# Optimization experiments

Hardware: AMD Instinct MI355X
Metric: run time of the kernel (lower is better)

Reference implementation:

```python
import jax, jax.numpy as jnp
import numpy as np

B, S, D, H = 4, 2048, 1024, 16
DK = D // H
THETA = 10000.0


def _rope(x, token_positions):
    # x: [b, h, s, d_k]; token_positions: [s] int
    half = x.shape[-1] // 2
    freqs = 1.0 / (THETA ** (2.0 * jnp.arange(half, dtype=jnp.float32) / x.shape[-1]))
    angles = token_positions.astype(jnp.float32)[:, None] * freqs[None, :]  # [s, half]
    cos, sin = jnp.cos(angles), jnp.sin(angles)
    x1 = x[..., 0::2]  # interleaved pairing: (d/2, 2)
    x2 = x[..., 1::2]
    r1 = x1 * cos - x2 * sin
    r2 = x2 * cos + x1 * sin
    return jnp.stack([r1, r2], axis=-1).reshape(x.shape)


def setup_inputs() -> dict:
    key = jax.random.key(0)
    ks = jax.random.split(key, 5)
    std_io = np.sqrt(2.0 / (D + D)).astype(np.float32)
    return {
        "x": jax.random.normal(ks[0], (B, S, D), dtype=jnp.float32),
        "token_positions": jnp.arange(S, dtype=jnp.int32),
        "Wq": jax.random.normal(ks[1], (D, D), dtype=jnp.float32) * std_io,
        "Wk": jax.random.normal(ks[2], (D, D), dtype=jnp.float32) * std_io,
        "Wv": jax.random.normal(ks[3], (D, D), dtype=jnp.float32) * std_io,
        "Wo": jax.random.normal(ks[4], (D, D), dtype=jnp.float32) * std_io,
    }


def reference(x, token_positions, Wq, Wk, Wv, Wo):
    b, s, d = x.shape
    # Linear uses W: [out, in] -> y = x @ W.T
    def proj(W):
        y = jnp.einsum('bsd,od->bso', x, W)
        return y.reshape(b, s, H, DK).transpose(0, 2, 1, 3)  # [b,h,s,dk]
    q, k, v = proj(Wq), proj(Wk), proj(Wv)
    q = _rope(q, token_positions)
    k = _rope(k, token_positions)
    scores = jnp.einsum('bhqd,bhkd->bhqk', q, k) / jnp.sqrt(jnp.float32(DK))
    causal = jnp.tril(jnp.ones((s, s), dtype=bool))
    scores = jnp.where(causal, scores, -jnp.inf)
    attn = jax.nn.softmax(scores, axis=-1)
    out = jnp.einsum('bhqk,bhkd->bhqd', attn, v)
    out = out.transpose(0, 2, 1, 3).reshape(b, s, d)
    return jnp.einsum('bsd,od->bso', out, Wo)
```

## Files before the change

### kernel.cpp

```cpp
#include <hip/hip_runtime.h>
#include <math.h>

#define B_ 4
#define S_ 2048
#define D_ 1024
#define H_ 16
#define DK_ 64
#define SCALE_ 0.125f
#define THETA_ 10000.0f
#define LOG2E_ 1.44269504f
#define THR_ 8.0f

typedef unsigned short ushort_t;
typedef __attribute__((ext_vector_type(8))) short bf16x8;
typedef __attribute__((ext_vector_type(4))) float f32x4;

__device__ __forceinline__ ushort_t f2bf(float f) {
    union { float f; unsigned u; } v; v.f = f;
    unsigned r = (v.u + 0x7FFFu + ((v.u >> 16) & 1u)) >> 16;
    return (ushort_t)r;
}

__device__ __forceinline__ unsigned permpk(float lo, float hi) {
    return __builtin_amdgcn_perm(__float_as_uint(hi), __float_as_uint(lo), 0x07060302u);
}

__device__ __forceinline__ int vswz(int row) { return (row & 7) ^ ((row >> 3) & 3); }

#define GLOAD_LDS16(gptr, lptr)                                                   \
    __builtin_amdgcn_global_load_lds(                                             \
        (const __attribute__((address_space(1))) unsigned int*)(gptr),            \
        (__attribute__((address_space(3))) unsigned int*)(lptr), 16, 0, 0)

__global__ __launch_bounds__(256) void cast_f32_bf16(const float* __restrict__ in,
                                                     ushort_t* __restrict__ out, int n) {
    int i = (blockIdx.x * 256 + threadIdx.x) * 4;
    if (i >= n) return;
    float4 v = *reinterpret_cast<const float4*>(in + i);
    unsigned lo = (unsigned)f2bf(v.x) | ((unsigned)f2bf(v.y) << 16);
    unsigned hi = (unsigned)f2bf(v.z) | ((unsigned)f2bf(v.w) << 16);
    uint2 u; u.x = lo; u.y = hi;
    *reinterpret_cast<uint2*>(out + i) = u;
}

__global__ __launch_bounds__(256) void build_rope(const int* __restrict__ pos,
                                                  float2* __restrict__ tab) {
    int i = blockIdx.x * 256 + threadIdx.x;
    int s = i >> 5, p = i & 31;
    float freq = powf(THETA_, -2.0f * (float)p / 64.0f);
    float a = (float)pos[s] * freq;
    tab[i] = make_float2(cosf(a), sinf(a));
}

template <int MODE>
__global__ __launch_bounds__(256) void gemm_bf16(const ushort_t* __restrict__ A,
                                                 const ushort_t* __restrict__ W,
                                                 const float2* __restrict__ tab,
                                                 float qscale,
                                                 float* __restrict__ outF,
                                                 ushort_t* __restrict__ outB) {
    __shared__ ushort_t Asl[128 * 32];
    __shared__ ushort_t Bsl[128 * 32];

    const int t = threadIdx.x;
    const int lane = t & 63;
    const int w = t >> 6;
    const int lr = lane & 15;
    const int lg = lane >> 4;

    const int bid = blockIdx.x;
    const int swz = (bid & 7) * 64 + (bid >> 3);
    const int m0 = (swz >> 3) * 128;
    const int n0 = (swz & 7) * 128;

    const int wr = w >> 1;
    const int wc = w & 1;

    f32x4 acc[4][4] = {};

    for (int k0 = 0; k0 < D_; k0 += 32) {
#pragma unroll
        for (int i = 0; i < 2; ++i) {
            const int off = w * 2048 + i * 1024 + lane * 16;
            const int row = off >> 6;
            const int col = (off & 63) >> 1;
            GLOAD_LDS16(A + (size_t)(m0 + row) * D_ + k0 + col, Asl + (w * 1024 + i * 512));
            GLOAD_LDS16(W + (size_t)(n0 + row) * D_ + k0 + col, Bsl + (w * 1024 + i * 512));
        }
        __syncthreads();

        bf16x8 af[4], bfr[4];
#pragma unroll
        for (int x = 0; x < 4; ++x) {
            af[x]  = *reinterpret_cast<const bf16x8*>(&Asl[(wr * 64 + x * 16 + lr) * 32 + lg * 8]);
            bfr[x] = *reinterpret_cast<const bf16x8*>(&Bsl[(wc * 64 + x * 16 + lr) * 32 + lg * 8]);
        }
#pragma unroll
        for (int mi = 0; mi < 4; ++mi)
#pragma unroll
            for (int ni = 0; ni < 4; ++ni)
                acc[mi][ni] = __builtin_amdgcn_mfma_f32_16x16x32_bf16(af[mi], bfr[ni], acc[mi][ni], 0, 0, 0);
        __syncthreads();
    }

#pragma unroll
    for (int mi = 0; mi < 4; ++mi) {
#pragma unroll
        for (int r = 0; r < 4; ++r) {
            const int m = m0 + wr * 64 + mi * 16 + lg * 4 + r;
            const int bb = m >> 11;
            const int s = m & (S_ - 1);
#pragma unroll
            for (int ni = 0; ni < 4; ++ni) {
                const int n = n0 + wc * 64 + ni * 16 + lr;
                float v = acc[mi][ni][r];
                if (MODE == 0) {
                    outF[(size_t)m * D_ + n] = v;
                } else {
                    const int h = n >> 6, dk = n & 63;
                    if (MODE == 2) {
                        v *= qscale;
                        const float2 cs = tab[s * 32 + (dk >> 1)];
                        const float part = __shfl_xor(v, 1, 64);
                        v = (dk & 1) ? fmaf(v, cs.x, part * cs.y)
                                     : fmaf(v, cs.x, -part * cs.y);
                    }
                    outB[(((size_t)bb * H_ + h) * S_ + s) * DK_ + dk] = f2bf(v);
                }
            }
        }
    }
}

__global__ __launch_bounds__(256) void attn_mfma(const ushort_t* __restrict__ Q,
                                                 const ushort_t* __restrict__ K,
                                                 const ushort_t* __restrict__ V,
                                                 ushort_t* __restrict__ O) {
    __shared__ ushort_t Ks[2][64 * 64];
    __shared__ ushort_t Vt[64 * 64];
    __shared__ ushort_t Pl[64 * 64];

    const int t = threadIdx.x;
    const int lane = t & 63;
    const int w = t >> 6;
    const int lr = lane & 15;
    const int lg = lane >> 4;

    const int bid = blockIdx.x;
    const int swz = (bid & 7) * 128 + (bid >> 3);
    const int bh = swz >> 4;
    const int p  = swz & 15;

    const ushort_t* Kbase = K + (size_t)bh * S_ * DK_;
    const ushort_t* Vbase = V + (size_t)bh * S_ * DK_;
    const int bb = bh >> 4, h = bh & 15;

    const int dk8 = (t & 7) * 8;
    const int kv2 = (t >> 3) * 2;

    bf16x8 ones;
#pragma unroll
    for (int j = 0; j < 8; ++j) ones[j] = (short)0x3F80;

    bf16x8 vpre0, vpre1;

    for (int ph = 0; ph < 2; ++ph) {
        const int qt = ph ? (31 - p) : p;
        const int q0 = qt * 64;
        const int nt = qt + 1;

        const ushort_t* Qbase = Q + ((size_t)bh * S_ + q0 + w * 16) * DK_;
        bf16x8 qf[2];
#pragma unroll
        for (int kf = 0; kf < 2; ++kf)
            qf[kf] = *reinterpret_cast<const bf16x8*>(
                Qbase + (size_t)lr * DK_ + kf * 32 + lg * 8);

        f32x4 acc[4] = {};
        f32x4 accl = {};
        float mrow = -INFINITY;

#pragma unroll
        for (int it = 0; it < 2; ++it) {
            const int slotbase = w * 64 + it * 256;
            const int slot = slotbase + lane;
            const int row = slot >> 3;
            const int c16 = (slot & 7) ^ (row & 7);
            GLOAD_LDS16(Kbase + (size_t)row * DK_ + c16 * 8, &Ks[0][slotbase * 8]);
        }
        {
            const ushort_t* Vsrc = Vbase + (size_t)kv2 * DK_ + dk8;
            vpre0 = *reinterpret_cast<const bf16x8*>(Vsrc);
            vpre1 = *reinterpret_cast<const bf16x8*>(Vsrc + DK_);
        }
        __syncthreads();

        int cur = 0;
        for (int kt = 0; kt < nt; ++kt) {
            {
                const unsigned* aw = reinterpret_cast<const unsigned*>(&vpre0);
                const unsigned* bw = reinterpret_cast<const unsigned*>(&vpre1);
#pragma unroll
                for (int j = 0; j < 8; ++j) {
                    const int row = dk8 + j;
                    const unsigned sel = (j & 1) ? 0x07060302u : 0x05040100u;
                    const unsigned pk = __builtin_amdgcn_perm(bw[j >> 1], aw[j >> 1], sel);
                    *reinterpret_cast<unsigned*>(
                        (char*)Vt + row * 128 + ((kv2 * 2) ^ (vswz(row) << 4))) = pk;
                }
            }
            __syncthreads();

            if (kt + 1 < nt) {
                const ushort_t* Ksrc = Kbase + (size_t)(kt + 1) * 64 * DK_;
#pragma unroll
                for (int it = 0; it < 2; ++it) {
                    const int slotbase = w * 64 + it * 256;
                    const int slot = slotbase + lane;
                    const int row = slot >> 3;
                    const int c16 = (slot & 7) ^ (row & 7);
                    GLOAD_LDS16(Ksrc + (size_t)row * DK_ + c16 * 8, &Ks[cur ^ 1][slotbase * 8]);
                }
                const ushort_t* Vsrc = Vbase + (size_t)((kt + 1) * 64 + kv2) * DK_ + dk8;
                vpre0 = *reinterpret_cast<const bf16x8*>(Vsrc);
                vpre1 = *reinterpret_cast<const bf16x8*>(Vsrc + DK_);
            }

            bf16x8 kb[4][2];
#pragma unroll
            for (int nf = 0; nf < 4; ++nf)
#pragma unroll
                for (int kf = 0; kf < 2; ++kf)
                    kb[nf][kf] = *reinterpret_cast<const bf16x8*>(
                        (char*)Ks[cur] + (nf * 16 + lr) * 128 + (((kf * 4 + lg) ^ (lr & 7)) << 4));

            f32x4 sT[4];
#pragma unroll
            for (int nf = 0; nf < 4; ++nf) {
                f32x4 z = {};
                z = __builtin_amdgcn_mfma_f32_16x16x32_bf16(kb[nf][0], qf[0], z, 0, 0, 0);
                z = __builtin_amdgcn_mfma_f32_16x16x32_bf16(kb[nf][1], qf[1], z, 0, 0, 0);
                sT[nf] = z;
            }

            if (kt == nt - 1) {
                const int q = q0 + w * 16 + lr;
#pragma unroll
                for (int nf = 0; nf < 4; ++nf)
#pragma unroll
                    for (int r = 0; r < 4; ++r) {
                        const int kv = kt * 64 + nf * 16 + lg * 4 + r;
                        if (kv > q) sT[nf][r] = -INFINITY;
                    }
            }

            {
                float m4 = -INFINITY;
#pragma unroll
                for (int nf = 0; nf < 4; ++nf)
#pragma unroll
                    for (int r = 0; r < 4; ++r) m4 = fmaxf(m4, sT[nf][r]);
                m4 = fmaxf(m4, __shfl_xor(m4, 16, 64));
                m4 = fmaxf(m4, __shfl_xor(m4, 32, 64));
                if (m4 > mrow + THR_) {
                    const float corr = __builtin_amdgcn_exp2f(mrow - m4);
                    mrow = m4;
#pragma unroll
                    for (int r = 0; r < 4; ++r) accl[r] *= corr;
#pragma unroll
                    for (int df = 0; df < 4; ++df)
#pragma unroll
                        for (int r = 0; r < 4; ++r) acc[df][r] *= corr;
                }
            }

            const int prow = w * 16 + lr;
            char* prowp = (char*)Pl + prow * 128;
#pragma unroll
            for (int nf = 0; nf < 4; ++nf) {
                const float p0 = __builtin_amdgcn_exp2f(sT[nf][0] - mrow);
                const float p1 = __builtin_amdgcn_exp2f(sT[nf][1] - mrow);
                const float p2 = __builtin_amdgcn_exp2f(sT[nf][2] - mrow);
                const float p3 = __builtin_amdgcn_exp2f(sT[nf][3] - mrow);
                uint2 pk;
                pk.x = permpk(p0, p1);
                pk.y = permpk(p2, p3);
                const int chunk = (nf * 2 + (lg >> 1)) ^ (lr & 7);
                *reinterpret_cast<uint2*>(prowp + (chunk << 4) + (lg & 1) * 8) = pk;
            }

            bf16x8 pfr[2];
#pragma unroll
            for (int kf = 0; kf < 2; ++kf)
                pfr[kf] = *reinterpret_cast<const bf16x8*>(
                    (char*)Pl + prow * 128 + (((kf * 4 + lg) ^ (lr & 7)) << 4));

            bf16x8 vtf[4][2];
#pragma unroll
            for (int df = 0; df < 4; ++df)
#pragma unroll
                for (int kf = 0; kf < 2; ++kf)
                    vtf[df][kf] = *reinterpret_cast<const bf16x8*>(
                        (char*)Vt + (df * 16 + lr) * 128 + (((kf * 4 + lg) ^ vswz(df * 16 + lr)) << 4));

#pragma unroll
            for (int kf = 0; kf < 2; ++kf)
                accl = __builtin_amdgcn_mfma_f32_16x16x32_bf16(ones, pfr[kf], accl, 0, 0, 0);
#pragma unroll
            for (int df = 0; df < 4; ++df)
#pragma unroll
                for (int kf = 0; kf < 2; ++kf)
                    acc[df] = __builtin_amdgcn_mfma_f32_16x16x32_bf16(vtf[df][kf], pfr[kf], acc[df], 0, 0, 0);

            __syncthreads();
            cur ^= 1;
        }

        const float inv = 1.0f / accl[0];
        const int q = q0 + w * 16 + lr;
        ushort_t* Orow = O + ((size_t)bb * S_ + q) * D_ + h * DK_;
#pragma unroll
        for (int df = 0; df < 4; ++df) {
            unsigned lo = (unsigned)f2bf(acc[df][0] * inv) | ((unsigned)f2bf(acc[df][1] * inv) << 16);
            unsigned hi = (unsigned)f2bf(acc[df][2] * inv) | ((unsigned)f2bf(acc[df][3] * inv) << 16);
            *reinterpret_cast<unsigned*>(Orow + df * 16 + lg * 4)     = lo;
            *reinterpret_cast<unsigned*>(Orow + df * 16 + lg * 4 + 2) = hi;
        }
    }
}

extern "C" void kernel_launch(void* const* d_in, const int* in_sizes, int n_in,
                              void* d_out, int out_size, void* d_ws, size_t ws_size,
                              hipStream_t stream) {
    const float* x  = (const float*)d_in[0];
    const int*   tp = (const int*)d_in[1];
    const float* Wq = (const float*)d_in[2];
    const float* Wk = (const float*)d_in[3];
    const float* Wv = (const float*)d_in[4];
    const float* Wo = (const float*)d_in[5];
    float* out = (float*)d_out;

    char* ws = (char*)d_ws;
    ushort_t* Xb  = (ushort_t*)(ws);
    ushort_t* Wqb = (ushort_t*)(ws + (16ull << 20));
    ushort_t* Wkb = (ushort_t*)(ws + (18ull << 20));
    ushort_t* Wvb = (ushort_t*)(ws + (20ull << 20));
    ushort_t* Wob = (ushort_t*)(ws + (22ull << 20));
    ushort_t* Qb  = (ushort_t*)(ws + (24ull << 20));
    ushort_t* Kb  = (ushort_t*)(ws + (40ull << 20));
    ushort_t* Vb  = (ushort_t*)(ws + (56ull << 20));
    ushort_t* Ao  = (ushort_t*)(ws + (72ull << 20));
    float2*   tab = (float2*)(ws + (88ull << 20));

    const int NX = B_ * S_ * D_;
    const int NW = D_ * D_;
    cast_f32_bf16<<<NX / 1024, 256, 0, stream>>>(x, Xb, NX);
    cast_f32_bf16<<<NW / 1024, 256, 0, stream>>>(Wq, Wqb, NW);
    cast_f32_bf16<<<NW / 1024, 256, 0, stream>>>(Wk, Wkb, NW);
    cast_f32_bf16<<<NW / 1024, 256, 0, stream>>>(Wv, Wvb, NW);
    cast_f32_bf16<<<NW / 1024, 256, 0, stream>>>(Wo, Wob, NW);
    build_rope<<<(S_ * 32) / 256, 256, 0, stream>>>(tp, tab);

    gemm_bf16<2><<<512, 256, 0, stream>>>(Xb, Wqb, tab, SCALE_ * LOG2E_, nullptr, Qb);
    gemm_bf16<2><<<512, 256, 0, stream>>>(Xb, Wkb, tab, 1.0f, nullptr, Kb);
    gemm_bf16<1><<<512, 256, 0, stream>>>(Xb, Wvb, tab, 1.0f, nullptr, Vb);

    attn_mfma<<<1024, 256, 0, stream>>>(Qb, Kb, Vb, Ao);

    gemm_bf16<0><<<512, 256, 0, stream>>>(Ao, Wob, tab, 1.0f, out, nullptr);
}
```

Measured before the change: 213.3 us.

## Widen attention query tile to 128 rows with 512-thread blocks

The attention kernel now processes 128 query rows per block using 8 waves instead of 64 rows with 4 waves, so each K/V tile loaded into shared memory is reused by twice as many queries. The grid is halved, the pairing of causal tiles is rebalanced over 16 query tiles, and the causal mask now covers the last two KV tiles. This halves K/V global traffic per query, at the cost of larger blocks, a larger P buffer in shared memory, possibly lower occupancy, and half the threads idle during the V transpose.

```diff
diff --git a/kernel.cpp b/kernel.cpp
--- a/kernel.cpp
+++ b/kernel.cpp
@@ -132,13 +132,13 @@
     }
 }
 
-__global__ __launch_bounds__(256) void attn_mfma(const ushort_t* __restrict__ Q,
+__global__ __launch_bounds__(512) void attn_mfma(const ushort_t* __restrict__ Q,
                                                  const ushort_t* __restrict__ K,
                                                  const ushort_t* __restrict__ V,
                                                  ushort_t* __restrict__ O) {
     __shared__ ushort_t Ks[2][64 * 64];
     __shared__ ushort_t Vt[64 * 64];
-    __shared__ ushort_t Pl[64 * 64];
+    __shared__ ushort_t Pl[128 * 64];
 
     const int t = threadIdx.x;
     const int lane = t & 63;
@@ -147,16 +147,18 @@
     const int lg = lane >> 4;
 
     const int bid = blockIdx.x;
-    const int swz = (bid & 7) * 128 + (bid >> 3);
-    const int bh = swz >> 4;
-    const int p  = swz & 15;
+    const int swz = (bid & 7) * 64 + (bid >> 3);
+    const int bh = swz >> 3;
+    const int p  = swz & 7;
 
     const ushort_t* Kbase = K + (size_t)bh * S_ * DK_;
     const ushort_t* Vbase = V + (size_t)bh * S_ * DK_;
     const int bb = bh >> 4, h = bh & 15;
 
+    const int krow = t >> 3;
+    const int kc16 = (t & 7) ^ (krow & 7);
     const int dk8 = (t & 7) * 8;
-    const int kv2 = (t >> 3) * 2;
+    const int kv2 = ((t >> 3) & 31) * 2;
 
     bf16x8 ones;
 #pragma unroll
@@ -165,9 +167,9 @@
     bf16x8 vpre0, vpre1;
 
     for (int ph = 0; ph < 2; ++ph) {
-        const int qt = ph ? (31 - p) : p;
-        const int q0 = qt * 64;
-        const int nt = qt + 1;
+        const int qt = ph ? (15 - p) : p;
+        const int q0 = qt * 128;
+        const int nt = 2 * qt + 2;
 
         const ushort_t* Qbase = Q + ((size_t)bh * S_ + q0 + w * 16) * DK_;
         bf16x8 qf[2];
@@ -180,15 +182,8 @@
         f32x4 accl = {};
         float mrow = -INFINITY;
 
-#pragma unroll
-        for (int it = 0; it < 2; ++it) {
-            const int slotbase = w * 64 + it * 256;
-            const int slot = slotbase + lane;
-            const int row = slot >> 3;
-            const int c16 = (slot & 7) ^ (row & 7);
-            GLOAD_LDS16(Kbase + (size_t)row * DK_ + c16 * 8, &Ks[0][slotbase * 8]);
-        }
-        {
+        GLOAD_LDS16(Kbase + (size_t)krow * DK_ + kc16 * 8, &Ks[0][t * 8]);
+        if (t < 256) {
             const ushort_t* Vsrc = Vbase + (size_t)kv2 * DK_ + dk8;
             vpre0 = *reinterpret_cast<const bf16x8*>(Vsrc);
             vpre1 = *reinterpret_cast<const bf16x8*>(Vsrc + DK_);
@@ -197,7 +192,7 @@
 
         int cur = 0;
         for (int kt = 0; kt < nt; ++kt) {
-            {
+            if (t < 256) {
                 const unsigned* aw = reinterpret_cast<const unsigned*>(&vpre0);
                 const unsigned* bw = reinterpret_cast<const unsigned*>(&vpre1);
 #pragma unroll
@@ -213,17 +208,12 @@
 
             if (kt + 1 < nt) {
                 const ushort_t* Ksrc = Kbase + (size_t)(kt + 1) * 64 * DK_;
-#pragma unroll
-                for (int it = 0; it < 2; ++it) {
-                    const int slotbase = w * 64 + it * 256;
-                    const int slot = slotbase + lane;
-                    const int row = slot >> 3;
-                    const int c16 = (slot & 7) ^ (row & 7);
-                    GLOAD_LDS16(Ksrc + (size_t)row * DK_ + c16 * 8, &Ks[cur ^ 1][slotbase * 8]);
+                GLOAD_LDS16(Ksrc + (size_t)krow * DK_ + kc16 * 8, &Ks[cur ^ 1][t * 8]);
+                if (t < 256) {
+                    const ushort_t* Vsrc = Vbase + (size_t)((kt + 1) * 64 + kv2) * DK_ + dk8;
+                    vpre0 = *reinterpret_cast<const bf16x8*>(Vsrc);
+                    vpre1 = *reinterpret_cast<const bf16x8*>(Vsrc + DK_);
                 }
-                const ushort_t* Vsrc = Vbase + (size_t)((kt + 1) * 64 + kv2) * DK_ + dk8;
-                vpre0 = *reinterpret_cast<const bf16x8*>(Vsrc);
-                vpre1 = *reinterpret_cast<const bf16x8*>(Vsrc + DK_);
             }
 
             bf16x8 kb[4][2];
@@ -243,7 +233,7 @@
                 sT[nf] = z;
             }
 
-            if (kt == nt - 1) {
+            if (kt >= nt - 2) {
                 const int q = q0 + w * 16 + lr;
 #pragma unroll
                 for (int nf = 0; nf < 4; ++nf)
@@ -365,7 +355,7 @@
     gemm_bf16<2><<<512, 256, 0, stream>>>(Xb, Wkb, tab, 1.0f, nullptr, Kb);
     gemm_bf16<1><<<512, 256, 0, stream>>>(Xb, Wvb, tab, 1.0f, nullptr, Vb);
 
-    attn_mfma<<<1024, 256, 0, stream>>>(Qb, Kb, Vb, Ao);
+    attn_mfma<<<512, 512, 0, stream>>>(Qb, Kb, Vb, Ao);
 
     gemm_bf16<0><<<512, 256, 0, stream>>>(Ao, Wob, tab, 1.0f, out, nullptr);
 }
```

Result: faster. 196.2 us (-8.0%).
